# Optimization experiments

Measured on AMD Instinct MI355X. Metric: run time of the kernel, lower is better.

## Reference

```python
import jax, jax.numpy as jnp
import numpy as np

N = 10000
E = 320000

def leaky(x):
    return jnp.where(x >= 0, x, 0.01 * x)

def spmm(rows, cols, vals, dense):
    # sparse(N,N) @ dense(N,D) via gather + segment-sum
    return jax.ops.segment_sum(vals[:, None] * dense[cols], rows, num_segments=N)

def setup_inputs() -> dict:
    key = jax.random.key(0)
    ks = jax.random.split(key, 16)
    def xav(k, shp):
        std = float(np.sqrt(2.0 / (shp[0] + shp[1])))
        return jax.random.normal(k, shp, dtype=jnp.float32) * std
    return {
        "x": jax.random.normal(ks[0], (N, 512), dtype=jnp.float32),
        "adj_rows": jax.random.randint(ks[1], (E,), 0, N, dtype=jnp.int32),
        "adj_cols": jax.random.randint(ks[2], (E,), 0, N, dtype=jnp.int32),
        "adj_vals": jax.random.uniform(ks[3], (E,), dtype=jnp.float32),
        "W1": xav(ks[4], (512, 256)), "b1": jnp.zeros((256,), jnp.float32),
        "Wc1a": xav(ks[5], (256, 128)), "bc1a": jnp.zeros((128,), jnp.float32),
        "Wc1b": xav(ks[6], (128, 64)), "bc1b": jnp.zeros((64,), jnp.float32),
        "Wc2a": xav(ks[7], (64, 128)), "bc2a": jnp.zeros((128,), jnp.float32),
        "Wc2b": xav(ks[8], (128, 256)), "bc2b": jnp.zeros((256,), jnp.float32),
        "W6": xav(ks[9], (256, 512)), "b6": jnp.zeros((512,), jnp.float32),
    }

def reference(x, adj_rows, adj_cols, adj_vals, W1, b1, Wc1a, bc1a, Wc1b, bc1b,
              Wc2a, bc2a, Wc2b, bc2b, W6, b6):
    # encode (eval mode: dropout is identity)
    h = spmm(adj_rows, adj_cols, adj_vals, x @ W1) + b1   # gc1
    h = leaky(h)
    z = leaky(h @ Wc1a + bc1a) @ Wc1b + bc1b              # classifier1, [N,64]
    # inner-product decoder with identity activation -> dense NxN adjacency
    A = z @ z.T                                            # [N,N]
    # decode: classifier2 then gc6 applied with the DENSE reconstructed adj
    h2 = leaky(z @ Wc2a + bc2a) @ Wc2b + bc2b              # [N,256]
    h2 = leaky(h2)
    out = A @ (h2 @ W6) + b6                               # [N,512]
    return (out, z)
```

## Files before the change

kernel.cpp:

```cpp
#include <hip/hip_runtime.h>
#include <hip/hip_bf16.h>

#define NROWS 10000
#define KPAD  10240

typedef __attribute__((ext_vector_type(8))) short bf16x8;
typedef __attribute__((ext_vector_type(4))) float f32x4;

__device__ __forceinline__ float leaky_f(float x) { return x >= 0.f ? x : 0.01f * x; }

__device__ __forceinline__ unsigned short f2bf(float f) {
    union { float f; unsigned int u; } v; v.f = f;
    unsigned int r = v.u + 0x7fffu + ((v.u >> 16) & 1u);
    return (unsigned short)(r >> 16);
}
__device__ __forceinline__ float bf2f(unsigned short h) {
    union { unsigned int u; float f; } v; v.u = ((unsigned int)h) << 16;
    return v.f;
}

__global__ void conv_all(const float* __restrict__ x, const float* __restrict__ W1,
                         const float* __restrict__ Wc1a, const float* __restrict__ Wc1b,
                         const float* __restrict__ Wc2a, const float* __restrict__ Wc2b,
                         const float* __restrict__ W6,
                         unsigned short* __restrict__ XHI,
                         unsigned short* __restrict__ o1, unsigned short* __restrict__ o2,
                         unsigned short* __restrict__ o3, unsigned short* __restrict__ o4,
                         unsigned short* __restrict__ o5, unsigned short* __restrict__ o6,
                         int* __restrict__ counts, unsigned short* __restrict__ Zt,
                         unsigned short* __restrict__ MBt) {
    int gid = blockIdx.x * 256 + threadIdx.x;
    if (gid < 1280000) {
        float4 v = ((const float4*)x)[gid];
        ushort4 h;
        h.x = f2bf(v.x); h.y = f2bf(v.y); h.z = f2bf(v.z); h.w = f2bf(v.w);
        ((ushort4*)XHI)[gid] = h;
    } else if (gid < 1411072) {
        int i = gid - 1280000, k = i >> 8, n = i & 255;
        o1[n * 512 + k] = f2bf(W1[i]);
    } else if (gid < 1443840) {
        int i = gid - 1411072, k = i >> 7, n = i & 127;
        o2[n * 256 + k] = f2bf(Wc1a[i]);
    } else if (gid < 1452032) {
        int i = gid - 1443840, k = i >> 6, n = i & 63;
        o3[n * 128 + k] = f2bf(Wc1b[i]);
    } else if (gid < 1460224) {
        int i = gid - 1452032, k = i >> 7, n = i & 127;
        o4[n * 64 + k] = f2bf(Wc2a[i]);
    } else if (gid < 1492992) {
        int i = gid - 1460224, k = i >> 8, n = i & 255;
        o5[n * 128 + k] = f2bf(Wc2b[i]);
    } else if (gid < 1624064) {
        int i = gid - 1492992, k = i >> 9, n = i & 511;
        o6[n * 256 + k] = f2bf(W6[i]);
    } else if (gid < 1634064) {
        counts[gid - 1624064] = 0;
    } else if (gid < 1649424) {
        int i = gid - 1634064;
        Zt[(size_t)(i / 240) * KPAD + 10000 + (i % 240)] = 0;
    } else if (gid < 1772304) {
        int i = gid - 1649424;
        MBt[(size_t)(i / 240) * KPAD + 10000 + (i % 240)] = 0;
    }
}

__global__ void hist_kernel(const int* __restrict__ rows, int* __restrict__ counts, int E) {
    int i = blockIdx.x * blockDim.x + threadIdx.x;
    if (i < E) atomicAdd(&counts[rows[i]], 1);
}

__global__ __launch_bounds__(1024)
void scan_kernel(const int* __restrict__ counts, int* __restrict__ starts,
                 int* __restrict__ cursor, int n) {
    __shared__ int buf[1024];
    __shared__ int base_s;
    int tid = threadIdx.x;
    if (tid == 0) base_s = 0;
    __syncthreads();
    for (int c0 = 0; c0 < n; c0 += 1024) {
        int i = c0 + tid;
        int v = (i < n) ? counts[i] : 0;
        buf[tid] = v;
        __syncthreads();
        for (int off = 1; off < 1024; off <<= 1) {
            int t = (tid >= off) ? buf[tid - off] : 0;
            __syncthreads();
            buf[tid] += t;
            __syncthreads();
        }
        int incl = buf[tid];
        int base = base_s;
        __syncthreads();
        if (i < n) { int ex = base + incl - v; starts[i] = ex; cursor[i] = ex; }
        if (tid == 1023) base_s = base + buf[1023];
        __syncthreads();
    }
    if (tid == 0) starts[n] = base_s;
}

__global__ void scatter_kernel(const int* __restrict__ rows, const int* __restrict__ cols,
                               const float* __restrict__ vals, int* __restrict__ cursor,
                               int* __restrict__ cols_s, float* __restrict__ vals_s, int E) {
    int i = blockIdx.x * blockDim.x + threadIdx.x;
    if (i < E) {
        int pos = atomicAdd(&cursor[rows[i]], 1);
        cols_s[pos] = cols[i];
        vals_s[pos] = vals[i];
    }
}

__global__ __launch_bounds__(64)
void spmm_leaky_kernel(const int* __restrict__ starts, const int* __restrict__ cols_s,
                       const float* __restrict__ vals_s, const unsigned short* __restrict__ C1b,
                       const float* __restrict__ b1, unsigned short* __restrict__ Hb) {
    int r = blockIdx.x;
    int t = threadIdx.x;
    float4 a0 = ((const float4*)b1)[t];
    float4 a1 = {0.f, 0.f, 0.f, 0.f};
    int s = starts[r], e = starts[r + 1];
    int p = s;
    for (; p + 2 <= e; p += 2) {
        int c0 = cols_s[p], c1 = cols_s[p + 1];
        float v0 = vals_s[p], v1 = vals_s[p + 1];
        ushort4 s0 = ((const ushort4*)(C1b + (size_t)c0 * 256))[t];
        ushort4 s1 = ((const ushort4*)(C1b + (size_t)c1 * 256))[t];
        a0.x += v0 * bf2f(s0.x); a0.y += v0 * bf2f(s0.y);
        a0.z += v0 * bf2f(s0.z); a0.w += v0 * bf2f(s0.w);
        a1.x += v1 * bf2f(s1.x); a1.y += v1 * bf2f(s1.y);
        a1.z += v1 * bf2f(s1.z); a1.w += v1 * bf2f(s1.w);
    }
    if (p < e) {
        int c0 = cols_s[p];
        float v0 = vals_s[p];
        ushort4 s0 = ((const ushort4*)(C1b + (size_t)c0 * 256))[t];
        a0.x += v0 * bf2f(s0.x); a0.y += v0 * bf2f(s0.y);
        a0.z += v0 * bf2f(s0.z); a0.w += v0 * bf2f(s0.w);
    }
    ushort4 h;
    h.x = f2bf(leaky_f(a0.x + a1.x));
    h.y = f2bf(leaky_f(a0.y + a1.y));
    h.z = f2bf(leaky_f(a0.z + a1.z));
    h.w = f2bf(leaky_f(a0.w + a1.w));
    ((ushort4*)Hb)[(size_t)r * 64 + t] = h;
}

template<int ACT, int WF32, int WBF, int WTB>
__global__ __launch_bounds__(256)
void gemm_mfma(const unsigned short* __restrict__ A, const unsigned short* __restrict__ Bt,
               const float* __restrict__ bias, float* __restrict__ Cf,
               unsigned short* __restrict__ Cb, unsigned short* __restrict__ Ct,
               int ldt, int M, int N, int K) {
    __shared__ short sA[64][72];
    __shared__ short sB[64][72];
    const int bm = blockIdx.x * 64;
    const int bn = blockIdx.y * 64;
    const int tid = threadIdx.x;
    const int lane = tid & 63, wid = tid >> 6;
    const int wm = wid & 1, wn = wid >> 1;
    const int l15 = lane & 15, kg = lane >> 4;

    f32x4 acc[2][2];
#pragma unroll
    for (int i = 0; i < 2; i++)
#pragma unroll
        for (int j = 0; j < 2; j++) acc[i][j] = (f32x4){0.f, 0.f, 0.f, 0.f};

    for (int k0 = 0; k0 < K; k0 += 64) {
#pragma unroll
        for (int it = 0; it < 2; ++it) {
            int idx = tid + it * 256;
            int r = idx >> 3, s = idx & 7;
            int gm = bm + r;
            uint4 va = {0u, 0u, 0u, 0u};
            if (gm < M) va = *(const uint4*)(A + (size_t)gm * K + k0 + s * 8);
            *(uint4*)(&sA[r][s * 8]) = va;
            uint4 vb = *(const uint4*)(Bt + (size_t)(bn + r) * K + k0 + s * 8);
            *(uint4*)(&sB[r][s * 8]) = vb;
        }
        __syncthreads();
        bf16x8 a[2][2], b[2][2];
#pragma unroll
        for (int i = 0; i < 2; i++)
#pragma unroll
            for (int ks = 0; ks < 2; ++ks) {
                a[i][ks] = *(const bf16x8*)(&sA[wm * 32 + i * 16 + l15][kg * 8 + ks * 32]);
                b[i][ks] = *(const bf16x8*)(&sB[wn * 32 + i * 16 + l15][kg * 8 + ks * 32]);
            }
#pragma unroll
        for (int ks = 0; ks < 2; ++ks)
#pragma unroll
            for (int i = 0; i < 2; i++)
#pragma unroll
                for (int j = 0; j < 2; j++)
                    acc[i][j] = __builtin_amdgcn_mfma_f32_16x16x32_bf16(a[i][ks], b[j][ks], acc[i][j], 0, 0, 0);
        __syncthreads();
    }

#pragma unroll
    for (int i = 0; i < 2; i++) {
        int row0 = wm * 32 + i * 16 + kg * 4;
#pragma unroll
        for (int j = 0; j < 2; j++) {
            int col = bn + wn * 32 + j * 16 + l15;
            float bv = bias ? bias[col] : 0.f;
            ushort4 tw;
#pragma unroll
            for (int r = 0; r < 4; r++) {
                int grow = bm + row0 + r;
                float v = acc[i][j][r] + bv;
                if (ACT) v = leaky_f(v);
                if (WF32) { if (grow < M) Cf[(size_t)grow * N + col] = v; }
                if (WBF)  { if (grow < M) Cb[(size_t)grow * N + col] = f2bf(v); }
                if (WTB)  ((unsigned short*)&tw)[r] = f2bf(v);
            }
            if (WTB && (bm + row0) < M)
                *(ushort4*)(&Ct[(size_t)col * ldt + bm + row0]) = tw;
        }
    }
}

__global__ __launch_bounds__(256)
void fused_enc(const unsigned short* __restrict__ H,
               const unsigned short* __restrict__ Wa,
               const unsigned short* __restrict__ Wb,
               const float* __restrict__ ba, const float* __restrict__ bb,
               float* __restrict__ Zf, unsigned short* __restrict__ Zb,
               unsigned short* __restrict__ Zt, int M) {
    __shared__ short sA[64][72];
    __shared__ short sB[128][72];
    __shared__ short sT1[64][136];
    __shared__ short sWb[64][136];
    const int bm = blockIdx.x * 64;
    const int tid = threadIdx.x;
    const int lane = tid & 63, wid = tid >> 6;
    const int wm = wid & 1, wn = wid >> 1;
    const int l15 = lane & 15, kg = lane >> 4;

#pragma unroll
    for (int it = 0; it < 4; ++it) {
        int idx = tid + it * 256;
        int r = idx >> 4, s = idx & 15;
        *(uint4*)(&sWb[r][s * 8]) = *(const uint4*)(Wb + r * 128 + s * 8);
    }

    f32x4 accA[2][4];
#pragma unroll
    for (int i = 0; i < 2; i++)
#pragma unroll
        for (int j = 0; j < 4; j++) accA[i][j] = (f32x4){0.f, 0.f, 0.f, 0.f};

    for (int k0 = 0; k0 < 256; k0 += 64) {
#pragma unroll
        for (int it = 0; it < 2; ++it) {
            int idx = tid + it * 256;
            int r = idx >> 3, s = idx & 7;
            int gm = bm + r;
            uint4 va = {0u, 0u, 0u, 0u};
            if (gm < M) va = *(const uint4*)(H + (size_t)gm * 256 + k0 + s * 8);
            *(uint4*)(&sA[r][s * 8]) = va;
        }
#pragma unroll
        for (int it = 0; it < 4; ++it) {
            int idx = tid + it * 256;
            int r = idx >> 3, s = idx & 7;
            *(uint4*)(&sB[r][s * 8]) = *(const uint4*)(Wa + r * 256 + k0 + s * 8);
        }
        __syncthreads();
#pragma unroll
        for (int ks = 0; ks < 2; ++ks) {
            bf16x8 a[2], b[4];
#pragma unroll
            for (int i = 0; i < 2; i++)
                a[i] = *(const bf16x8*)(&sA[wm * 32 + i * 16 + l15][kg * 8 + ks * 32]);
#pragma unroll
            for (int j = 0; j < 4; j++)
                b[j] = *(const bf16x8*)(&sB[wn * 64 + j * 16 + l15][kg * 8 + ks * 32]);
#pragma unroll
            for (int i = 0; i < 2; i++)
#pragma unroll
                for (int j = 0; j < 4; j++)
                    accA[i][j] = __builtin_amdgcn_mfma_f32_16x16x32_bf16(a[i], b[j], accA[i][j], 0, 0, 0);
        }
        __syncthreads();
    }
#pragma unroll
    for (int i = 0; i < 2; i++) {
        int row0 = wm * 32 + i * 16 + kg * 4;
#pragma unroll
        for (int j = 0; j < 4; j++) {
            int col = wn * 64 + j * 16 + l15;
            float bv = ba[col];
#pragma unroll
            for (int r = 0; r < 4; r++)
                sT1[row0 + r][col] = f2bf(leaky_f(accA[i][j][r] + bv));
        }
    }
    __syncthreads();

    f32x4 accB[2][2];
#pragma unroll
    for (int i = 0; i < 2; i++)
#pragma unroll
        for (int j = 0; j < 2; j++) accB[i][j] = (f32x4){0.f, 0.f, 0.f, 0.f};
#pragma unroll
    for (int kc = 0; kc < 4; ++kc) {
        bf16x8 a[2], b[2];
#pragma unroll
        for (int i = 0; i < 2; i++)
            a[i] = *(const bf16x8*)(&sT1[wm * 32 + i * 16 + l15][kc * 32 + kg * 8]);
#pragma unroll
        for (int j = 0; j < 2; j++)
            b[j] = *(const bf16x8*)(&sWb[wn * 32 + j * 16 + l15][kc * 32 + kg * 8]);
#pragma unroll
        for (int i = 0; i < 2; i++)
#pragma unroll
            for (int j = 0; j < 2; j++)
                accB[i][j] = __builtin_amdgcn_mfma_f32_16x16x32_bf16(a[i], b[j], accB[i][j], 0, 0, 0);
    }
#pragma unroll
    for (int i = 0; i < 2; i++) {
        int row0 = wm * 32 + i * 16 + kg * 4;
#pragma unroll
        for (int j = 0; j < 2; j++) {
            int col = wn * 32 + j * 16 + l15;
            float bv = bb[col];
            ushort4 tw;
#pragma unroll
            for (int r = 0; r < 4; r++) {
                int grow = bm + row0 + r;
                float v = accB[i][j][r] + bv;
                if (grow < M) {
                    Zf[(size_t)grow * 64 + col] = v;
                    Zb[(size_t)grow * 64 + col] = f2bf(v);
                }
                ((unsigned short*)&tw)[r] = f2bf(v);
            }
            if ((bm + row0) < M)
                *(ushort4*)(&Zt[(size_t)col * KPAD + bm + row0]) = tw;
        }
    }
}

__global__ __launch_bounds__(256)
void fused_dec(const unsigned short* __restrict__ Z,
               const unsigned short* __restrict__ Wa,
               const unsigned short* __restrict__ Wb,
               const float* __restrict__ ba, const float* __restrict__ bb,
               unsigned short* __restrict__ H2, int M) {
    __shared__ short sA[64][72];
    __shared__ short sB[128][72];
    __shared__ short sT2[64][136];
    __shared__ short sB2[256][72];
    const int bm = blockIdx.x * 64;
    const int tid = threadIdx.x;
    const int lane = tid & 63, wid = tid >> 6;
    const int wm = wid & 1, wn = wid >> 1;
    const int l15 = lane & 15, kg = lane >> 4;

#pragma unroll
    for (int it = 0; it < 2; ++it) {
        int idx = tid + it * 256;
        int r = idx >> 3, s = idx & 7;
        int gm = bm + r;
        uint4 va = {0u, 0u, 0u, 0u};
        if (gm < M) va = *(const uint4*)(Z + (size_t)gm * 64 + s * 8);
        *(uint4*)(&sA[r][s * 8]) = va;
    }
#pragma unroll
    for (int it = 0; it < 4; ++it) {
        int idx = tid + it * 256;
        int r = idx >> 3, s = idx & 7;
        *(uint4*)(&sB[r][s * 8]) = *(const uint4*)(Wa + r * 64 + s * 8);
    }
    __syncthreads();
    f32x4 accA[2][4];
#pragma unroll
    for (int i = 0; i < 2; i++)
#pragma unroll
        for (int j = 0; j < 4; j++) accA[i][j] = (f32x4){0.f, 0.f, 0.f, 0.f};
#pragma unroll
    for (int ks = 0; ks < 2; ++ks) {
        bf16x8 a[2], b[4];
#pragma unroll
        for (int i = 0; i < 2; i++)
            a[i] = *(const bf16x8*)(&sA[wm * 32 + i * 16 + l15][kg * 8 + ks * 32]);
#pragma unroll
        for (int j = 0; j < 4; j++)
            b[j] = *(const bf16x8*)(&sB[wn * 64 + j * 16 + l15][kg * 8 + ks * 32]);
#pragma unroll
        for (int i = 0; i < 2; i++)
#pragma unroll
            for (int j = 0; j < 4; j++)
                accA[i][j] = __builtin_amdgcn_mfma_f32_16x16x32_bf16(a[i], b[j], accA[i][j], 0, 0, 0);
    }
    __syncthreads();
#pragma unroll
    for (int i = 0; i < 2; i++) {
        int row0 = wm * 32 + i * 16 + kg * 4;
#pragma unroll
        for (int j = 0; j < 4; j++) {
            int col = wn * 64 + j * 16 + l15;
            float bv = ba[col];
#pragma unroll
            for (int r = 0; r < 4; r++)
                sT2[row0 + r][col] = f2bf(leaky_f(accA[i][j][r] + bv));
        }
    }
    __syncthreads();

    f32x4 accB[2][8];
#pragma unroll
    for (int i = 0; i < 2; i++)
#pragma unroll
        for (int j = 0; j < 8; j++) accB[i][j] = (f32x4){0.f, 0.f, 0.f, 0.f};
    for (int k0 = 0; k0 < 128; k0 += 64) {
#pragma unroll
        for (int it = 0; it < 8; ++it) {
            int idx = tid + it * 256;
            int r = idx >> 3, s = idx & 7;
            *(uint4*)(&sB2[r][s * 8]) = *(const uint4*)(Wb + r * 128 + k0 + s * 8);
        }
        __syncthreads();
#pragma unroll
        for (int ks = 0; ks < 2; ++ks) {
            bf16x8 a[2], b[8];
#pragma unroll
            for (int i = 0; i < 2; i++)
                a[i] = *(const bf16x8*)(&sT2[wm * 32 + i * 16 + l15][k0 + ks * 32 + kg * 8]);
#pragma unroll
            for (int j = 0; j < 8; j++)
                b[j] = *(const bf16x8*)(&sB2[wn * 128 + j * 16 + l15][kg * 8 + ks * 32]);
#pragma unroll
            for (int i = 0; i < 2; i++)
#pragma unroll
                for (int j = 0; j < 8; j++)
                    accB[i][j] = __builtin_amdgcn_mfma_f32_16x16x32_bf16(a[i], b[j], accB[i][j], 0, 0, 0);
        }
        __syncthreads();
    }
#pragma unroll
    for (int i = 0; i < 2; i++) {
        int row0 = wm * 32 + i * 16 + kg * 4;
#pragma unroll
        for (int j = 0; j < 8; j++) {
            int col = wn * 128 + j * 16 + l15;
            float bv = bb[col];
#pragma unroll
            for (int r = 0; r < 4; r++) {
                int grow = bm + row0 + r;
                if (grow < M)
                    H2[(size_t)grow * 256 + col] = f2bf(leaky_f(accB[i][j][r] + bv));
            }
        }
    }
}

__global__ __launch_bounds__(256)
void sgemm_sk(const unsigned short* __restrict__ Zt, const unsigned short* __restrict__ MBt,
              float* __restrict__ part) {
    __shared__ short sA[64][72];
    __shared__ short sB[64][72];
    const int bn = blockIdx.x * 64;
    const int kc = blockIdx.y;
    const int tid = threadIdx.x;
    const int lane = tid & 63, wid = tid >> 6;
    const int wm = wid & 1, wn = wid >> 1;
    const int l15 = lane & 15, kg = lane >> 4;

    f32x4 acc[2][2];
#pragma unroll
    for (int i = 0; i < 2; i++)
#pragma unroll
        for (int j = 0; j < 2; j++) acc[i][j] = (f32x4){0.f, 0.f, 0.f, 0.f};

    for (int kk = 0; kk < 4; ++kk) {
        int k0 = kc * 256 + kk * 64;
#pragma unroll
        for (int it = 0; it < 2; ++it) {
            int idx = tid + it * 256;
            int r = idx >> 3, s = idx & 7;
            *(uint4*)(&sA[r][s * 8]) = *(const uint4*)(Zt + (size_t)r * KPAD + k0 + s * 8);
            *(uint4*)(&sB[r][s * 8]) = *(const uint4*)(MBt + (size_t)(bn + r) * KPAD + k0 + s * 8);
        }
        __syncthreads();
        bf16x8 a[2][2], b[2][2];
#pragma unroll
        for (int i = 0; i < 2; i++)
#pragma unroll
            for (int ks = 0; ks < 2; ++ks) {
                a[i][ks] = *(const bf16x8*)(&sA[wm * 32 + i * 16 + l15][kg * 8 + ks * 32]);
                b[i][ks] = *(const bf16x8*)(&sB[wn * 32 + i * 16 + l15][kg * 8 + ks * 32]);
            }
#pragma unroll
        for (int ks = 0; ks < 2; ++ks)
#pragma unroll
            for (int i = 0; i < 2; i++)
#pragma unroll
                for (int j = 0; j < 2; j++)
                    acc[i][j] = __builtin_amdgcn_mfma_f32_16x16x32_bf16(a[i][ks], b[j][ks], acc[i][j], 0, 0, 0);
        __syncthreads();
    }
#pragma unroll
    for (int i = 0; i < 2; i++) {
        int row0 = wm * 32 + i * 16 + kg * 4;
#pragma unroll
        for (int j = 0; j < 2; j++) {
            int col = bn + wn * 32 + j * 16 + l15;
#pragma unroll
            for (int r = 0; r < 4; r++)
                part[((size_t)kc * 64 + row0 + r) * 512 + col] = acc[i][j][r];
        }
    }
}

__global__ void reduce_S(const float* __restrict__ part, unsigned short* __restrict__ Stb) {
    int i = blockIdx.x * blockDim.x + threadIdx.x;
    if (i < 64 * 512) {
        float s = 0.f;
#pragma unroll
        for (int c = 0; c < 40; ++c) s += part[(size_t)c * (64 * 512) + i];
        int k = i >> 9, n = i & 511;
        Stb[(size_t)n * 64 + k] = f2bf(s);
    }
}

extern "C" void kernel_launch(void* const* d_in, const int* in_sizes, int n_in,
                              void* d_out, int out_size, void* d_ws, size_t ws_size,
                              hipStream_t stream) {
    const float* x    = (const float*)d_in[0];
    const int*   rows = (const int*)d_in[1];
    const int*   cols = (const int*)d_in[2];
    const float* vals = (const float*)d_in[3];
    const float* W1   = (const float*)d_in[4];
    const float* b1   = (const float*)d_in[5];
    const float* Wc1a = (const float*)d_in[6];
    const float* bc1a = (const float*)d_in[7];
    const float* Wc1b = (const float*)d_in[8];
    const float* bc1b = (const float*)d_in[9];
    const float* Wc2a = (const float*)d_in[10];
    const float* bc2a = (const float*)d_in[11];
    const float* Wc2b = (const float*)d_in[12];
    const float* bc2b = (const float*)d_in[13];
    const float* W6   = (const float*)d_in[14];
    const float* b6   = (const float*)d_in[15];

    const int N = NROWS;
    const int E = in_sizes[1];

    float* ws = (float*)d_ws;
    unsigned short* XHI  = (unsigned short*)(ws + 0);
    unsigned short* C1b  = (unsigned short*)(ws + 2560000);
    unsigned short* HHI  = (unsigned short*)(ws + 3840000);
    unsigned short* ZHI  = (unsigned short*)(ws + 5120000);
    unsigned short* ZT   = (unsigned short*)(ws + 5440000);
    unsigned short* MBt  = (unsigned short*)(ws + 5767680);
    float*          PART = ws + 8389120;
    unsigned short* STB  = (unsigned short*)(ws + 9699840);
    unsigned short* W1T   = (unsigned short*)(ws + 9716224);
    unsigned short* WC1AT = (unsigned short*)(ws + 9781760);
    unsigned short* WC1BT = (unsigned short*)(ws + 9798144);
    unsigned short* WC2AT = (unsigned short*)(ws + 9802240);
    unsigned short* WC2BT = (unsigned short*)(ws + 9806336);
    unsigned short* W6T   = (unsigned short*)(ws + 9822720);
    unsigned short* H2HI  = HHI;

    int*   counts = (int*)(ws + 9888256);
    int*   starts = counts + 10000;
    int*   cursor = starts + 10001;
    int*   cols_s = cursor + 10000;
    float* vals_s = (float*)(cols_s + 320000);

    float* Out = (float*)d_out;
    float* Zp  = (float*)d_out + 5120000;

    const int GX = (N + 63) / 64;

    conv_all<<<6924, 256, 0, stream>>>(x, W1, Wc1a, Wc1b, Wc2a, Wc2b, W6, XHI,
                                       W1T, WC1AT, WC1BT, WC2AT, WC2BT, W6T,
                                       counts, ZT, MBt);

    hist_kernel<<<(E + 255) / 256, 256, 0, stream>>>(rows, counts, E);
    scan_kernel<<<1, 1024, 0, stream>>>(counts, starts, cursor, N);
    scatter_kernel<<<(E + 255) / 256, 256, 0, stream>>>(rows, cols, vals, cursor, cols_s, vals_s, E);

    gemm_mfma<0,0,1,0><<<dim3(GX, 4), 256, 0, stream>>>(XHI, W1T, nullptr,
                                                        nullptr, C1b, nullptr, 0, N, 256, 512);
    spmm_leaky_kernel<<<N, 64, 0, stream>>>(starts, cols_s, vals_s, C1b, b1, HHI);

    fused_enc<<<GX, 256, 0, stream>>>(HHI, WC1AT, WC1BT, bc1a, bc1b, Zp, ZHI, ZT, N);

    fused_dec<<<GX, 256, 0, stream>>>(ZHI, WC2AT, WC2BT, bc2a, bc2b, H2HI, N);

    gemm_mfma<0,0,0,1><<<dim3(GX, 8), 256, 0, stream>>>(H2HI, W6T, nullptr,
                                                        nullptr, nullptr, MBt, KPAD, N, 512, 256);
    sgemm_sk<<<dim3(8, 40), 256, 0, stream>>>(ZT, MBt, PART);
    reduce_S<<<128, 256, 0, stream>>>(PART, STB);

    gemm_mfma<0,1,0,0><<<dim3(GX, 8), 256, 0, stream>>>(ZHI, STB, b6,
                                                        Out, nullptr, nullptr, 0, N, 512, 64);
}
```

Measured before the change: 158.9 us.

## Reassociate decoder as Z·((Zᵀ·H2)·W6) and tune scan and SpMM unrolling

```diff
diff --git a/kernel.cpp b/kernel.cpp
--- a/kernel.cpp
+++ b/kernel.cpp
@@ -28,7 +28,7 @@
                          unsigned short* __restrict__ o3, unsigned short* __restrict__ o4,
                          unsigned short* __restrict__ o5, unsigned short* __restrict__ o6,
                          int* __restrict__ counts, unsigned short* __restrict__ Zt,
-                         unsigned short* __restrict__ MBt) {
+                         unsigned short* __restrict__ H2t) {
     int gid = blockIdx.x * 256 + threadIdx.x;
     if (gid < 1280000) {
         float4 v = ((const float4*)x)[gid];
@@ -58,9 +58,9 @@
     } else if (gid < 1649424) {
         int i = gid - 1634064;
         Zt[(size_t)(i / 240) * KPAD + 10000 + (i % 240)] = 0;
-    } else if (gid < 1772304) {
+    } else if (gid < 1710864) {
         int i = gid - 1649424;
-        MBt[(size_t)(i / 240) * KPAD + 10000 + (i % 240)] = 0;
+        H2t[(size_t)(i / 240) * KPAD + 10000 + (i % 240)] = 0;
     }
 }
 
@@ -73,29 +73,31 @@
 void scan_kernel(const int* __restrict__ counts, int* __restrict__ starts,
                  int* __restrict__ cursor, int n) {
     __shared__ int buf[1024];
-    __shared__ int base_s;
     int tid = threadIdx.x;
-    if (tid == 0) base_s = 0;
+    int base = tid * 10;
+    int v[10];
+    int local = 0;
+#pragma unroll
+    for (int j = 0; j < 10; ++j) {
+        int i = base + j;
+        v[j] = (i < n) ? counts[i] : 0;
+        local += v[j];
+    }
+    buf[tid] = local;
     __syncthreads();
-    for (int c0 = 0; c0 < n; c0 += 1024) {
-        int i = c0 + tid;
-        int v = (i < n) ? counts[i] : 0;
-        buf[tid] = v;
-        __syncthreads();
-        for (int off = 1; off < 1024; off <<= 1) {
-            int t = (tid >= off) ? buf[tid - off] : 0;
-            __syncthreads();
-            buf[tid] += t;
-            __syncthreads();
-        }
-        int incl = buf[tid];
-        int base = base_s;
-        __syncthreads();
-        if (i < n) { int ex = base + incl - v; starts[i] = ex; cursor[i] = ex; }
-        if (tid == 1023) base_s = base + buf[1023];
-        __syncthreads();
-    }
-    if (tid == 0) starts[n] = base_s;
+    for (int off = 1; off < 1024; off <<= 1) {
+        int t = (tid >= off) ? buf[tid - off] : 0;
+        __syncthreads();
+        buf[tid] += t;
+        __syncthreads();
+    }
+    int run = buf[tid] - local;
+#pragma unroll
+    for (int j = 0; j < 10; ++j) {
+        int i = base + j;
+        if (i < n) { starts[i] = run; cursor[i] = run; run += v[j]; }
+    }
+    if (tid == 1023) starts[n] = buf[1023];
 }
 
 __global__ void scatter_kernel(const int* __restrict__ rows, const int* __restrict__ cols,
@@ -117,19 +119,27 @@
     int t = threadIdx.x;
     float4 a0 = ((const float4*)b1)[t];
     float4 a1 = {0.f, 0.f, 0.f, 0.f};
+    float4 a2 = {0.f, 0.f, 0.f, 0.f};
+    float4 a3 = {0.f, 0.f, 0.f, 0.f};
     int s = starts[r], e = starts[r + 1];
     int p = s;
-    for (; p + 2 <= e; p += 2) {
-        int c0 = cols_s[p], c1 = cols_s[p + 1];
-        float v0 = vals_s[p], v1 = vals_s[p + 1];
+    for (; p + 4 <= e; p += 4) {
+        int c0 = cols_s[p], c1 = cols_s[p + 1], c2 = cols_s[p + 2], c3 = cols_s[p + 3];
+        float v0 = vals_s[p], v1 = vals_s[p + 1], v2 = vals_s[p + 2], v3 = vals_s[p + 3];
         ushort4 s0 = ((const ushort4*)(C1b + (size_t)c0 * 256))[t];
         ushort4 s1 = ((const ushort4*)(C1b + (size_t)c1 * 256))[t];
+        ushort4 s2 = ((const ushort4*)(C1b + (size_t)c2 * 256))[t];
+        ushort4 s3 = ((const ushort4*)(C1b + (size_t)c3 * 256))[t];
         a0.x += v0 * bf2f(s0.x); a0.y += v0 * bf2f(s0.y);
         a0.z += v0 * bf2f(s0.z); a0.w += v0 * bf2f(s0.w);
         a1.x += v1 * bf2f(s1.x); a1.y += v1 * bf2f(s1.y);
         a1.z += v1 * bf2f(s1.z); a1.w += v1 * bf2f(s1.w);
-    }
-    if (p < e) {
+        a2.x += v2 * bf2f(s2.x); a2.y += v2 * bf2f(s2.y);
+        a2.z += v2 * bf2f(s2.z); a2.w += v2 * bf2f(s2.w);
+        a3.x += v3 * bf2f(s3.x); a3.y += v3 * bf2f(s3.y);
+        a3.z += v3 * bf2f(s3.z); a3.w += v3 * bf2f(s3.w);
+    }
+    for (; p < e; ++p) {
         int c0 = cols_s[p];
         float v0 = vals_s[p];
         ushort4 s0 = ((const ushort4*)(C1b + (size_t)c0 * 256))[t];
@@ -137,10 +147,10 @@
         a0.z += v0 * bf2f(s0.z); a0.w += v0 * bf2f(s0.w);
     }
     ushort4 h;
-    h.x = f2bf(leaky_f(a0.x + a1.x));
-    h.y = f2bf(leaky_f(a0.y + a1.y));
-    h.z = f2bf(leaky_f(a0.z + a1.z));
-    h.w = f2bf(leaky_f(a0.w + a1.w));
+    h.x = f2bf(leaky_f(a0.x + a1.x + a2.x + a3.x));
+    h.y = f2bf(leaky_f(a0.y + a1.y + a2.y + a3.y));
+    h.z = f2bf(leaky_f(a0.z + a1.z + a2.z + a3.z));
+    h.w = f2bf(leaky_f(a0.w + a1.w + a2.w + a3.w));
     ((ushort4*)Hb)[(size_t)r * 64 + t] = h;
 }
 
@@ -346,7 +356,7 @@
                const unsigned short* __restrict__ Wa,
                const unsigned short* __restrict__ Wb,
                const float* __restrict__ ba, const float* __restrict__ bb,
-               unsigned short* __restrict__ H2, int M) {
+               unsigned short* __restrict__ H2t, int M) {
     __shared__ short sA[64][72];
     __shared__ short sB[128][72];
     __shared__ short sT2[64][136];
@@ -445,18 +455,18 @@
         for (int j = 0; j < 8; j++) {
             int col = wn * 128 + j * 16 + l15;
             float bv = bb[col];
-#pragma unroll
-            for (int r = 0; r < 4; r++) {
-                int grow = bm + row0 + r;
-                if (grow < M)
-                    H2[(size_t)grow * 256 + col] = f2bf(leaky_f(accB[i][j][r] + bv));
-            }
+            ushort4 tw;
+#pragma unroll
+            for (int r = 0; r < 4; r++)
+                ((unsigned short*)&tw)[r] = f2bf(leaky_f(accB[i][j][r] + bv));
+            if ((bm + row0) < M)
+                *(ushort4*)(&H2t[(size_t)col * KPAD + bm + row0]) = tw;
         }
     }
 }
 
 __global__ __launch_bounds__(256)
-void sgemm_sk(const unsigned short* __restrict__ Zt, const unsigned short* __restrict__ MBt,
+void sgemm_sk(const unsigned short* __restrict__ Zt, const unsigned short* __restrict__ H2t,
               float* __restrict__ part) {
     __shared__ short sA[64][72];
     __shared__ short sB[64][72];
@@ -480,7 +490,7 @@
             int idx = tid + it * 256;
             int r = idx >> 3, s = idx & 7;
             *(uint4*)(&sA[r][s * 8]) = *(const uint4*)(Zt + (size_t)r * KPAD + k0 + s * 8);
-            *(uint4*)(&sB[r][s * 8]) = *(const uint4*)(MBt + (size_t)(bn + r) * KPAD + k0 + s * 8);
+            *(uint4*)(&sB[r][s * 8]) = *(const uint4*)(H2t + (size_t)(bn + r) * KPAD + k0 + s * 8);
         }
         __syncthreads();
         bf16x8 a[2][2], b[2][2];
@@ -508,19 +518,18 @@
             int col = bn + wn * 32 + j * 16 + l15;
 #pragma unroll
             for (int r = 0; r < 4; r++)
-                part[((size_t)kc * 64 + row0 + r) * 512 + col] = acc[i][j][r];
-        }
-    }
-}
-
-__global__ void reduce_S(const float* __restrict__ part, unsigned short* __restrict__ Stb) {
+                part[((size_t)kc * 64 + row0 + r) * 256 + col] = acc[i][j][r];
+        }
+    }
+}
+
+__global__ void reduce_S2(const float* __restrict__ part, unsigned short* __restrict__ S2b) {
     int i = blockIdx.x * blockDim.x + threadIdx.x;
-    if (i < 64 * 512) {
+    if (i < 64 * 256) {
         float s = 0.f;
 #pragma unroll
-        for (int c = 0; c < 40; ++c) s += part[(size_t)c * (64 * 512) + i];
-        int k = i >> 9, n = i & 511;
-        Stb[(size_t)n * 64 + k] = f2bf(s);
+        for (int c = 0; c < 40; ++c) s += part[(size_t)c * (64 * 256) + i];
+        S2b[i] = f2bf(s);
     }
 }
 
@@ -553,18 +562,18 @@
     unsigned short* HHI  = (unsigned short*)(ws + 3840000);
     unsigned short* ZHI  = (unsigned short*)(ws + 5120000);
     unsigned short* ZT   = (unsigned short*)(ws + 5440000);
-    unsigned short* MBt  = (unsigned short*)(ws + 5767680);
-    float*          PART = ws + 8389120;
-    unsigned short* STB  = (unsigned short*)(ws + 9699840);
-    unsigned short* W1T   = (unsigned short*)(ws + 9716224);
-    unsigned short* WC1AT = (unsigned short*)(ws + 9781760);
-    unsigned short* WC1BT = (unsigned short*)(ws + 9798144);
-    unsigned short* WC2AT = (unsigned short*)(ws + 9802240);
-    unsigned short* WC2BT = (unsigned short*)(ws + 9806336);
-    unsigned short* W6T   = (unsigned short*)(ws + 9822720);
-    unsigned short* H2HI  = HHI;
-
-    int*   counts = (int*)(ws + 9888256);
+    unsigned short* H2T  = (unsigned short*)(ws + 5767680);
+    float*          PART = ws + 7078400;
+    unsigned short* S2B  = (unsigned short*)(ws + 7733760);
+    unsigned short* W6ST = (unsigned short*)(ws + 7741952);
+    unsigned short* W1T   = (unsigned short*)(ws + 7758336);
+    unsigned short* WC1AT = (unsigned short*)(ws + 7823872);
+    unsigned short* WC1BT = (unsigned short*)(ws + 7840256);
+    unsigned short* WC2AT = (unsigned short*)(ws + 7844352);
+    unsigned short* WC2BT = (unsigned short*)(ws + 7848448);
+    unsigned short* W6T   = (unsigned short*)(ws + 7864832);
+
+    int*   counts = (int*)(ws + 7930368);
     int*   starts = counts + 10000;
     int*   cursor = starts + 10001;
     int*   cols_s = cursor + 10000;
@@ -575,9 +584,9 @@
 
     const int GX = (N + 63) / 64;
 
-    conv_all<<<6924, 256, 0, stream>>>(x, W1, Wc1a, Wc1b, Wc2a, Wc2b, W6, XHI,
+    conv_all<<<6683, 256, 0, stream>>>(x, W1, Wc1a, Wc1b, Wc2a, Wc2b, W6, XHI,
                                        W1T, WC1AT, WC1BT, WC2AT, WC2BT, W6T,
-                                       counts, ZT, MBt);
+                                       counts, ZT, H2T);
 
     hist_kernel<<<(E + 255) / 256, 256, 0, stream>>>(rows, counts, E);
     scan_kernel<<<1, 1024, 0, stream>>>(counts, starts, cursor, N);
@@ -589,13 +598,14 @@
 
     fused_enc<<<GX, 256, 0, stream>>>(HHI, WC1AT, WC1BT, bc1a, bc1b, Zp, ZHI, ZT, N);
 
-    fused_dec<<<GX, 256, 0, stream>>>(ZHI, WC2AT, WC2BT, bc2a, bc2b, H2HI, N);
-
-    gemm_mfma<0,0,0,1><<<dim3(GX, 8), 256, 0, stream>>>(H2HI, W6T, nullptr,
-                                                        nullptr, nullptr, MBt, KPAD, N, 512, 256);
-    sgemm_sk<<<dim3(8, 40), 256, 0, stream>>>(ZT, MBt, PART);
-    reduce_S<<<128, 256, 0, stream>>>(PART, STB);
-
-    gemm_mfma<0,1,0,0><<<dim3(GX, 8), 256, 0, stream>>>(ZHI, STB, b6,
+    fused_dec<<<GX, 256, 0, stream>>>(ZHI, WC2AT, WC2BT, bc2a, bc2b, H2T, N);
+
+    sgemm_sk<<<dim3(4, 40), 256, 0, stream>>>(ZT, H2T, PART);
+    reduce_S2<<<64, 256, 0, stream>>>(PART, S2B);
+
+    gemm_mfma<0,0,0,1><<<dim3(1, 8), 256, 0, stream>>>(S2B, W6T, nullptr,
+                                                       nullptr, nullptr, W6ST, 64, 64, 512, 256);
+
+    gemm_mfma<0,1,0,0><<<dim3(GX, 8), 256, 0, stream>>>(ZHI, W6ST, b6,
                                                         Out, nullptr, nullptr, 0, N, 512, 64);
 }
```

Measured after the change: 135.6 us. 1.17x faster.
